# Kernel optimization log

Measured on AMD Instinct MI355X. Metric: run time of the kernel, lower is better.

## Reference

```python
import jax, jax.numpy as jnp
import numpy as np

H = 32        # query heads
HKV = 8       # kv heads
D = 64        # head_dim
EPS = 1e-6    # rms_norm_eps
LAYER_IDX = 8
LAMBDA_INIT = float(0.8 - 0.6 * np.exp(-0.3 * LAYER_IDX))
NEG = -1e9


def rotate_half(x):
    x1, x2 = jnp.split(x, 2, axis=-1)
    return jnp.concatenate([-x2, x1], axis=-1)


def setup_inputs() -> dict:
    key = jax.random.key(0)
    ks = jax.random.split(key, 10)
    B, S, HID = 1, 2048, 2048
    hidden_states = jax.random.normal(ks[0], (B, S, HID), jnp.float32)
    # rotary embeddings (HF llama style): cos/sin [S, D]
    inv_freq = 1.0 / (10000.0 ** (np.arange(0, D, 2, dtype=np.float64) / D))
    freqs = np.outer(np.arange(S, dtype=np.float64), inv_freq)
    emb = np.concatenate([freqs, freqs], axis=-1)
    cos = jnp.asarray(np.cos(emb), jnp.float32)
    sin = jnp.asarray(np.sin(emb), jnp.float32)
    w = 0.02
    Wq = w * jax.random.normal(ks[1], (H * D, HID), jnp.float32)
    Wk = w * jax.random.normal(ks[2], (HKV * D, HID), jnp.float32)
    Wv = w * jax.random.normal(ks[3], (HKV * D, HID), jnp.float32)
    Wo = w * jax.random.normal(ks[4], (HID, H * D), jnp.float32)
    lam_std = 0.1
    lambda_q1 = lam_std * jax.random.normal(ks[5], (D,), jnp.float32)
    lambda_k1 = lam_std * jax.random.normal(ks[6], (D,), jnp.float32)
    lambda_q2 = lam_std * jax.random.normal(ks[7], (D,), jnp.float32)
    lambda_k2 = lam_std * jax.random.normal(ks[8], (D,), jnp.float32)
    return dict(hidden_states=hidden_states, cos=cos, sin=sin, Wq=Wq, Wk=Wk,
                Wv=Wv, Wo=Wo, lambda_q1=lambda_q1, lambda_k1=lambda_k1,
                lambda_q2=lambda_q2, lambda_k2=lambda_k2)


def reference(hidden_states, cos, sin, Wq, Wk, Wv, Wo,
              lambda_q1, lambda_k1, lambda_q2, lambda_k2):
    B, S, _ = hidden_states.shape
    # projections -> [B, H, S, D]
    q = (hidden_states @ Wq.T).reshape(B, S, H, D).transpose(0, 2, 1, 3)
    k = (hidden_states @ Wk.T).reshape(B, S, HKV, D).transpose(0, 2, 1, 3)
    v = (hidden_states @ Wv.T).reshape(B, S, HKV, D).transpose(0, 2, 1, 3)
    # RoPE (cos/sin broadcast over batch/head dims)
    q = q * cos + rotate_half(q) * sin
    k = k * cos + rotate_half(k) * sin
    # GQA repeat_kv: each kv head repeated consecutively
    g = H // HKV
    k = jnp.repeat(k, g, axis=1)
    v = jnp.repeat(v, g, axis=1)
    # differential value: concat first/second half of heads along feature dim
    v_cat = jnp.concatenate([v[:, :H // 2], v[:, H // 2:]], axis=-1)  # [B,H/2,S,2D]
    v_rep = jnp.tile(v_cat, (1, 2, 1, 1))                              # [B,H,S,2D]
    # causal attention (flash-attn is_causal, dropout=0 at eval)
    scores = jnp.einsum('bhqd,bhkd->bhqk', q, k) / np.sqrt(D)
    causal = jnp.tril(jnp.ones((S, S), bool))
    scores = jnp.where(causal, scores, NEG)
    probs = jax.nn.softmax(scores.astype(jnp.float32), axis=-1).astype(q.dtype)
    out = jnp.einsum('bhqk,bhkd->bhqd', probs, v_rep)  # [B,H,S,2D]
    out1, out2 = out[:, :H // 2], out[:, H // 2:]
    lam1 = jnp.exp(jnp.sum(lambda_q1 * lambda_k1))
    lam2 = jnp.exp(jnp.sum(lambda_q2 * lambda_k2))
    lam = lam1 - lam2 + LAMBDA_INIT
    a = out1 - lam * out2                               # [B,H/2,S,2D]
    # RMSNorm over 2D, no affine
    a = a * jax.lax.rsqrt(jnp.mean(a * a, axis=-1, keepdims=True) + EPS)
    a = (1.0 - LAMBDA_INIT) * a
    a = a.transpose(0, 2, 1, 3).reshape(B, S, H * D)
    return a @ Wo.T
```

## Files before the change

kernel.cpp:

```cpp
#include <hip/hip_runtime.h>

typedef unsigned short u16;
typedef __attribute__((ext_vector_type(8))) short v8s;
typedef __attribute__((ext_vector_type(4))) float v4f;

#define S_LEN 2048
#define HID   2048
#define NH    32
#define NKV   8
#define HD    64
#define DVV   128
#define LAMBDA_INIT  0.7455692280263525f
#define ONE_MINUS_LI 0.2544307719736475f

__device__ __forceinline__ u16 f2b(float f){
  union { float f; unsigned int i; } v; v.f = f;
  unsigned int x = v.i;
  unsigned int r = (x + 0x7fffu + ((x >> 16) & 1u)) >> 16;
  return (u16)r;
}
__device__ __forceinline__ float b2f(u16 u){
  union { unsigned int i; float f; } v; v.i = ((unsigned int)u) << 16; return v.f;
}

__device__ __forceinline__ void gld16(const u16* g, u16* l){
  __builtin_amdgcn_global_load_lds(
      (const __attribute__((address_space(1))) unsigned int*)g,
      (__attribute__((address_space(3))) unsigned int*)l, 16, 0, 0);
}

__global__ __launch_bounds__(256) void cast5(
    const float* __restrict__ hs, const float* __restrict__ Wq,
    const float* __restrict__ Wk, const float* __restrict__ Wv,
    const float* __restrict__ Wo,
    u16* __restrict__ hsb, u16* __restrict__ Wqkvb, u16* __restrict__ Wob)
{
  int b = blockIdx.x;
  const float* S; u16* D; int rb;
  if (b < 2048)      { S = hs; D = hsb;             rb = b; }
  else if (b < 4096) { S = Wq; D = Wqkvb;           rb = b - 2048; }
  else if (b < 4608) { S = Wk; D = Wqkvb + 4194304; rb = b - 4096; }
  else if (b < 5120) { S = Wv; D = Wqkvb + 5242880; rb = b - 4608; }
  else               { S = Wo; D = Wob;             rb = b - 5120; }
  size_t i = ((size_t)rb * 256 + threadIdx.x) * 8;
  float4 a = *(const float4*)(S + i);
  float4 c = *(const float4*)(S + i + 4);
  u16 o[8] = {f2b(a.x), f2b(a.y), f2b(a.z), f2b(a.w), f2b(c.x), f2b(c.y), f2b(c.z), f2b(c.w)};
  *(uint4*)(D + i) = *(const uint4*)o;
}

template<int OUT_BF16>
__global__ __launch_bounds__(256) void gemm_bf16(const u16* __restrict__ A, const u16* __restrict__ B,
                                                 void* __restrict__ Cv, int M, int N, int K)
{
  __shared__ __attribute__((aligned(16))) u16 As[128*64];
  __shared__ __attribute__((aligned(16))) u16 Bs[128*64];
  const int t    = threadIdx.x;
  const int w    = t >> 6, lane = t & 63;
  const int mm   = lane & 15, g = lane >> 4;
  const int wr   = w >> 1, wc = w & 1;
  const int m0   = blockIdx.y * 128, n0 = blockIdx.x * 128;
  const int srow = w*32 + (lane >> 3);
  const int sch  = lane & 7;

  v4f acc[4][4];
#pragma unroll
  for (int i = 0; i < 4; i++)
#pragma unroll
    for (int j = 0; j < 4; j++) acc[i][j] = (v4f){0.f,0.f,0.f,0.f};

  for (int k0 = 0; k0 < K; k0 += 64){
    __syncthreads();
#pragma unroll
    for (int i = 0; i < 4; i++){
      int r  = srow + i*8;
      int ce = ((sch ^ (r & 7)) * 8);
      gld16(A + (size_t)(m0 + r) * K + k0 + ce, &As[w*2048 + i*512]);
      gld16(B + (size_t)(n0 + r) * K + k0 + ce, &Bs[w*2048 + i*512]);
    }
    __syncthreads();
#pragma unroll
    for (int kc = 0; kc < 2; kc++){
      v8s af[4], bf[4];
#pragma unroll
      for (int i = 0; i < 4; i++){
        int r = wr*64 + i*16 + mm;
        af[i] = *(const v8s*)&As[r*64 + (((kc*4 + g) ^ (r & 7)) * 8)];
      }
#pragma unroll
      for (int j = 0; j < 4; j++){
        int r = wc*64 + j*16 + mm;
        bf[j] = *(const v8s*)&Bs[r*64 + (((kc*4 + g) ^ (r & 7)) * 8)];
      }
#pragma unroll
      for (int i = 0; i < 4; i++)
#pragma unroll
        for (int j = 0; j < 4; j++)
          acc[i][j] = __builtin_amdgcn_mfma_f32_16x16x32_bf16(af[i], bf[j], acc[i][j], 0, 0, 0);
    }
  }
  if (OUT_BF16){
    u16* C = (u16*)Cv;
#pragma unroll
    for (int i = 0; i < 4; i++)
#pragma unroll
      for (int j = 0; j < 4; j++)
#pragma unroll
        for (int r = 0; r < 4; r++)
          C[(size_t)(m0 + wr*64 + i*16 + g*4 + r) * N + n0 + wc*64 + j*16 + mm] = f2b(acc[i][j][r]);
  } else {
    float* C = (float*)Cv;
#pragma unroll
    for (int i = 0; i < 4; i++)
#pragma unroll
      for (int j = 0; j < 4; j++)
#pragma unroll
        for (int r = 0; r < 4; r++)
          C[(size_t)(m0 + wr*64 + i*16 + g*4 + r) * N + n0 + wc*64 + j*16 + mm] = acc[i][j][r];
  }
}

__global__ __launch_bounds__(256) void rope_all(const u16* __restrict__ QKVb,
    const float* __restrict__ cosb, const float* __restrict__ sinb,
    u16* __restrict__ Qbf, u16* __restrict__ Kbf)
{
  int b = blockIdx.x;
  int d, h, s;
  const u16* src; u16* dst;
  if (b < 8192){
    int idx = b * 256 + threadIdx.x;
    d = idx & 31; h = (idx >> 5) & 31; s = idx >> 10;
    src = QKVb + (size_t)s * 3072 + h * HD + d;
    dst = Qbf + ((size_t)h * S_LEN + s) * HD + d;
  } else {
    int idx = (b - 8192) * 256 + threadIdx.x;
    d = idx & 31; h = (idx >> 5) & 7; s = idx >> 8;
    src = QKVb + (size_t)s * 3072 + 2048 + h * HD + d;
    dst = Kbf + ((size_t)h * S_LEN + s) * HD + d;
  }
  float c1 = cosb[s * HD + d],      s1 = sinb[s * HD + d];
  float c2 = cosb[s * HD + d + 32], s2 = sinb[s * HD + d + 32];
  float x1 = b2f(src[0]), x2 = b2f(src[32]);
  dst[0]  = f2b(x1 * c1 - x2 * s1);
  dst[32] = f2b(x2 * c2 + x1 * s2);
}

__global__ __launch_bounds__(256) void vtrans(const u16* __restrict__ Vb, int stride, u16* __restrict__ Vt)
{
  __shared__ u16 T[64][72];
  const int b = blockIdx.x;
  const int h = b >> 5;
  const int s0 = (b & 31) * 64;
  const int t = threadIdx.x;
#pragma unroll
  for (int i = 0; i < 4; i++){
    int u = t + i * 256;
    int r = u >> 4, c4 = (u & 15) * 4;
    uint2 v = *(const uint2*)&Vb[(size_t)(s0 + r) * stride + h * HD + c4];
    T[c4+0][r] = (u16)(v.x & 0xffff); T[c4+1][r] = (u16)(v.x >> 16);
    T[c4+2][r] = (u16)(v.y & 0xffff); T[c4+3][r] = (u16)(v.y >> 16);
  }
  __syncthreads();
#pragma unroll
  for (int i = 0; i < 2; i++){
    int u = t + i * 256;
    int d = u >> 3, ch = (u & 7) * 8;
    *(uint4*)&Vt[((size_t)h * HD + d) * S_LEN + s0 + ch] = *(const uint4*)&T[d][ch];
  }
}

__global__ __launch_bounds__(512) void attn_fused(
    const u16* __restrict__ Qbf, const u16* __restrict__ Kbf, const u16* __restrict__ Vt,
    const float* __restrict__ lq1, const float* __restrict__ lk1,
    const float* __restrict__ lq2, const float* __restrict__ lk2,
    u16* __restrict__ Ctx)
{
  __shared__ __attribute__((aligned(16))) u16 SM[41984];
  u16* QPa = SM;
  u16* QPb = SM + 4608;
  u16* Ksf = SM + 9216;
  u16* Vs  = SM + 25600;
  float* OLDS = (float*)(SM + 9216);

  const int p   = blockIdx.x;
  const int hp  = blockIdx.y;
  const int kva = hp >> 2, kvb = kva + 4;
  const int t   = threadIdx.x, w = t >> 6, lane = t & 63;
  const int hb  = w >> 2;
  const int wq  = w & 3;
  const int mm  = lane & 15, g = lane >> 4, g8 = g * 8;
  const int sr  = t >> 3;
  const int sc  = t & 7;
  const int so  = sc * 8;
  const int x0  = ((g ^ (mm & 7)) * 8);
  const int x1  = (((g + 4) ^ (mm & 7)) * 8);

  u16* QP = hb ? QPb : QPa;

  float lp1 = lq1[lane] * lk1[lane];
  float lp2 = lq2[lane] * lk2[lane];
#pragma unroll
  for (int off = 1; off < 64; off <<= 1){
    lp1 += __shfl_xor(lp1, off);
    lp2 += __shfl_xor(lp2, off);
  }
  const float lam = __expf(lp1) - __expf(lp2) + LAMBDA_INIT;

  for (int seg = 0; seg < 2; seg++){
    const int qt = seg ? p : (31 - p);
    const int q0 = qt * 64;

    __syncthreads();
    {
      int ce = ((sc ^ (sr & 7)) * 8);
      gld16(Kbf + ((size_t)kva * S_LEN + sr) * HD + ce, Ksf + (w*8)*64);
      gld16(Kbf + ((size_t)kvb * S_LEN + sr) * HD + ce, Ksf + 8192 + (w*8)*64);
      gld16(Vt + ((size_t)kva * HD + sr) * S_LEN + ce, Vs + (w*8)*64);
      gld16(Vt + ((size_t)kvb * HD + sr) * S_LEN + ce, Vs + (w*8 + 64)*64);
    }
    *(uint4*)&QPa[sr*72 + so] = *(const uint4*)&Qbf[((size_t)hp        * S_LEN + q0 + sr) * HD + so];
    *(uint4*)&QPb[sr*72 + so] = *(const uint4*)&Qbf[((size_t)(hp + 16) * S_LEN + q0 + sr) * HD + so];
    __syncthreads();
    v8s qa0 = *(const v8s*)&QP[(wq*16 + mm)*72 + g8];
    v8s qa1 = *(const v8s*)&QP[(wq*16 + mm)*72 + 32 + g8];

    v4f O[8];
#pragma unroll
    for (int n = 0; n < 8; n++) O[n] = (v4f){0.f,0.f,0.f,0.f};
    float l[4] = {0.f,0.f,0.f,0.f};

    for (int k0 = 0; k0 <= q0; k0 += 64){
      const int cur = (k0 >> 6) & 1;
      if (k0){
        asm volatile("s_waitcnt vmcnt(0)" ::: "memory");
        __builtin_amdgcn_s_barrier();
        __builtin_amdgcn_sched_barrier(0);
      }
      if (k0 + 64 <= q0){
        int ce = ((sc ^ (sr & 7)) * 8);
        gld16(Vt + ((size_t)kva * HD + sr) * S_LEN + k0 + 64 + ce, Vs + (cur^1)*8192 + (w*8)*64);
        gld16(Vt + ((size_t)kvb * HD + sr) * S_LEN + k0 + 64 + ce, Vs + (cur^1)*8192 + (w*8 + 64)*64);
        gld16(Kbf + ((size_t)kva * S_LEN + k0 + 64 + sr) * HD + ce, Ksf + (cur^1)*4096 + (w*8)*64);
        gld16(Kbf + ((size_t)kvb * S_LEN + k0 + 64 + sr) * HD + ce, Ksf + 8192 + (cur^1)*4096 + (w*8)*64);
      }

      const u16* Kh = Ksf + hb*8192 + cur*4096;
      const bool dg = (k0 == q0);
      v4f S[4];
#pragma unroll
      for (int n = 0; n < 4; n++){
        int row = n*16 + mm;
        v8s kb0 = *(const v8s*)&Kh[row*64 + x0];
        v8s kb1 = *(const v8s*)&Kh[row*64 + x1];
        v4f z = (v4f){0.f,0.f,0.f,0.f};
        z = __builtin_amdgcn_mfma_f32_16x16x32_bf16(qa0, kb0, z, 0, 0, 0);
        z = __builtin_amdgcn_mfma_f32_16x16x32_bf16(qa1, kb1, z, 0, 0, 0);
        S[n] = z;
      }
#pragma unroll
      for (int n = 0; n < 4; n++)
#pragma unroll
        for (int r = 0; r < 4; r++){
          float pe = __expf(S[n][r] * 0.125f);
          if (dg && (n*16 + mm > wq*16 + g*4 + r)) pe = 0.f;
          l[r] += pe;
          QP[(wq*16 + g*4 + r)*72 + n*16 + mm] = f2b(pe);
        }
      v8s pa0 = *(const v8s*)&QP[(wq*16 + mm)*72 + g8];
      v8s pa1 = *(const v8s*)&QP[(wq*16 + mm)*72 + 32 + g8];
      const u16* Vh = Vs + cur*8192;
#pragma unroll
      for (int n = 0; n < 8; n++){
        int row = n*16 + mm;
        v8s vb0 = *(const v8s*)&Vh[row*64 + x0];
        v8s vb1 = *(const v8s*)&Vh[row*64 + x1];
        O[n] = __builtin_amdgcn_mfma_f32_16x16x32_bf16(pa0, vb0, O[n], 0, 0, 0);
        O[n] = __builtin_amdgcn_mfma_f32_16x16x32_bf16(pa1, vb1, O[n], 0, 0, 0);
      }
    }

#pragma unroll
    for (int off = 1; off < 16; off <<= 1)
#pragma unroll
      for (int r = 0; r < 4; r++)
        l[r] += __shfl_xor(l[r], off);
    float il[4];
#pragma unroll
    for (int r = 0; r < 4; r++) il[r] = hb ? (lam / l[r]) : (1.0f / l[r]);

    __syncthreads();
    if (hb){
#pragma unroll
      for (int n = 0; n < 8; n++)
#pragma unroll
        for (int r = 0; r < 4; r++)
          OLDS[(wq*16 + g*4 + r)*128 + n*16 + mm] = O[n][r] * il[r];
    }
    __syncthreads();
    if (!hb){
      float av[8][4];
      float ss[4] = {0.f,0.f,0.f,0.f};
#pragma unroll
      for (int n = 0; n < 8; n++)
#pragma unroll
        for (int r = 0; r < 4; r++){
          float a = O[n][r] * il[r] - OLDS[(wq*16 + g*4 + r)*128 + n*16 + mm];
          av[n][r] = a;
          ss[r] += a * a;
        }
#pragma unroll
      for (int off = 1; off < 16; off <<= 1)
#pragma unroll
        for (int r = 0; r < 4; r++)
          ss[r] += __shfl_xor(ss[r], off);
      float rv[4];
#pragma unroll
      for (int r = 0; r < 4; r++)
        rv[r] = rsqrtf(ss[r] * (1.0f/128.0f) + 1e-6f) * ONE_MINUS_LI;
#pragma unroll
      for (int n = 0; n < 8; n++)
#pragma unroll
        for (int r = 0; r < 4; r++){
          int srow = q0 + wq*16 + g*4 + r;
          Ctx[(size_t)srow * HID + hp * DVV + n*16 + mm] = f2b(av[n][r] * rv[r]);
        }
    }
  }
}

extern "C" void kernel_launch(void* const* d_in, const int* in_sizes, int n_in,
                              void* d_out, int out_size, void* d_ws, size_t ws_size,
                              hipStream_t stream)
{
  (void)in_sizes; (void)n_in; (void)out_size; (void)ws_size;
  const float* hs   = (const float*)d_in[0];
  const float* cosb = (const float*)d_in[1];
  const float* sinb = (const float*)d_in[2];
  const float* Wq   = (const float*)d_in[3];
  const float* Wk   = (const float*)d_in[4];
  const float* Wv   = (const float*)d_in[5];
  const float* Wo   = (const float*)d_in[6];
  const float* lq1  = (const float*)d_in[7];
  const float* lk1  = (const float*)d_in[8];
  const float* lq2  = (const float*)d_in[9];
  const float* lk2  = (const float*)d_in[10];

  char* ws = (char*)d_ws;
  u16* hsb   = (u16*)(ws);
  u16* Wqkvb = (u16*)(ws + (8u  << 20));
  u16* QKVb  = (u16*)(ws + (20u << 20));
  u16* Ctx   = (u16*)(ws + (20u << 20));
  u16* Wob   = (u16*)(ws + (32u << 20));
  u16* Kbf   = (u16*)(ws + (44u << 20));
  u16* Vt    = (u16*)(ws + (46u << 20));
  u16* Qbf   = (u16*)(ws + (48u << 20));

  cast5<<<7168, 256, 0, stream>>>(hs, Wq, Wk, Wv, Wo, hsb, Wqkvb, Wob);
  gemm_bf16<1><<<dim3(24, 16), 256, 0, stream>>>(hsb, Wqkvb, QKVb, S_LEN, 3072, HID);
  rope_all<<<10240, 256, 0, stream>>>(QKVb, cosb, sinb, Qbf, Kbf);
  vtrans<<<NKV * (S_LEN/64), 256, 0, stream>>>(QKVb + 2560, 3072, Vt);
  attn_fused<<<dim3(16, 16), 512, 0, stream>>>(Qbf, Kbf, Vt, lq1, lk1, lq2, lk2, Ctx);
  gemm_bf16<0><<<dim3(16, 16), 256, 0, stream>>>(Ctx, Wob, (float*)d_out, S_LEN, 2048, HID);
}
```

Measured before the change: 253.6 us.

## Replace paired query-tile scheduling with 128-row tiles using 1024-thread blocks

```diff
diff --git a/kernel.cpp b/kernel.cpp
--- a/kernel.cpp
+++ b/kernel.cpp
@@ -169,31 +169,36 @@
   }
 }
 
-__global__ __launch_bounds__(512) void attn_fused(
+__global__ __launch_bounds__(1024, 4) void attn_fused(
     const u16* __restrict__ Qbf, const u16* __restrict__ Kbf, const u16* __restrict__ Vt,
     const float* __restrict__ lq1, const float* __restrict__ lk1,
     const float* __restrict__ lq2, const float* __restrict__ lk2,
     u16* __restrict__ Ctx)
 {
-  __shared__ __attribute__((aligned(16))) u16 SM[41984];
+  __shared__ __attribute__((aligned(16))) u16 SM[51200];
   u16* QPa = SM;
-  u16* QPb = SM + 4608;
-  u16* Ksf = SM + 9216;
-  u16* Vs  = SM + 25600;
-  float* OLDS = (float*)(SM + 9216);
-
-  const int p   = blockIdx.x;
+  u16* QPb = SM + 9216;
+  u16* Ksf = SM + 18432;
+  u16* Vs  = SM + 34816;
+  float* OLDS = (float*)(SM + 18432);
+
+  const int d   = blockIdx.x;
   const int hp  = blockIdx.y;
   const int kva = hp >> 2, kvb = kva + 4;
   const int t   = threadIdx.x, w = t >> 6, lane = t & 63;
-  const int hb  = w >> 2;
-  const int wq  = w & 3;
+  const int hb  = w >> 3;
+  const int wq  = w & 7;
   const int mm  = lane & 15, g = lane >> 4, g8 = g * 8;
   const int sr  = t >> 3;
   const int sc  = t & 7;
   const int so  = sc * 8;
   const int x0  = ((g ^ (mm & 7)) * 8);
   const int x1  = (((g + 4) ^ (mm & 7)) * 8);
+  const int khd  = (sr >> 6) ? kvb : kva;
+  const int rloc = sr & 63;
+  const int ce   = ((sc ^ (sr & 7)) * 8);
+  u16* kdst = Ksf + (w >> 3) * 8192 + ((w & 7) * 8) * 64;
+  u16* vdst = Vs + (w * 8) * 64;
 
   u16* QP = hb ? QPb : QPa;
 
@@ -206,125 +211,115 @@
   }
   const float lam = __expf(lp1) - __expf(lp2) + LAMBDA_INIT;
 
-  for (int seg = 0; seg < 2; seg++){
-    const int qt = seg ? p : (31 - p);
-    const int q0 = qt * 64;
-
-    __syncthreads();
-    {
-      int ce = ((sc ^ (sr & 7)) * 8);
-      gld16(Kbf + ((size_t)kva * S_LEN + sr) * HD + ce, Ksf + (w*8)*64);
-      gld16(Kbf + ((size_t)kvb * S_LEN + sr) * HD + ce, Ksf + 8192 + (w*8)*64);
-      gld16(Vt + ((size_t)kva * HD + sr) * S_LEN + ce, Vs + (w*8)*64);
-      gld16(Vt + ((size_t)kvb * HD + sr) * S_LEN + ce, Vs + (w*8 + 64)*64);
-    }
-    *(uint4*)&QPa[sr*72 + so] = *(const uint4*)&Qbf[((size_t)hp        * S_LEN + q0 + sr) * HD + so];
-    *(uint4*)&QPb[sr*72 + so] = *(const uint4*)&Qbf[((size_t)(hp + 16) * S_LEN + q0 + sr) * HD + so];
-    __syncthreads();
-    v8s qa0 = *(const v8s*)&QP[(wq*16 + mm)*72 + g8];
-    v8s qa1 = *(const v8s*)&QP[(wq*16 + mm)*72 + 32 + g8];
-
-    v4f O[8];
-#pragma unroll
-    for (int n = 0; n < 8; n++) O[n] = (v4f){0.f,0.f,0.f,0.f};
-    float l[4] = {0.f,0.f,0.f,0.f};
-
-    for (int k0 = 0; k0 <= q0; k0 += 64){
-      const int cur = (k0 >> 6) & 1;
-      if (k0){
-        asm volatile("s_waitcnt vmcnt(0)" ::: "memory");
-        __builtin_amdgcn_s_barrier();
-        __builtin_amdgcn_sched_barrier(0);
-      }
-      if (k0 + 64 <= q0){
-        int ce = ((sc ^ (sr & 7)) * 8);
-        gld16(Vt + ((size_t)kva * HD + sr) * S_LEN + k0 + 64 + ce, Vs + (cur^1)*8192 + (w*8)*64);
-        gld16(Vt + ((size_t)kvb * HD + sr) * S_LEN + k0 + 64 + ce, Vs + (cur^1)*8192 + (w*8 + 64)*64);
-        gld16(Kbf + ((size_t)kva * S_LEN + k0 + 64 + sr) * HD + ce, Ksf + (cur^1)*4096 + (w*8)*64);
-        gld16(Kbf + ((size_t)kvb * S_LEN + k0 + 64 + sr) * HD + ce, Ksf + 8192 + (cur^1)*4096 + (w*8)*64);
-      }
-
-      const u16* Kh = Ksf + hb*8192 + cur*4096;
-      const bool dg = (k0 == q0);
-      v4f S[4];
-#pragma unroll
-      for (int n = 0; n < 4; n++){
-        int row = n*16 + mm;
-        v8s kb0 = *(const v8s*)&Kh[row*64 + x0];
-        v8s kb1 = *(const v8s*)&Kh[row*64 + x1];
-        v4f z = (v4f){0.f,0.f,0.f,0.f};
-        z = __builtin_amdgcn_mfma_f32_16x16x32_bf16(qa0, kb0, z, 0, 0, 0);
-        z = __builtin_amdgcn_mfma_f32_16x16x32_bf16(qa1, kb1, z, 0, 0, 0);
-        S[n] = z;
-      }
-#pragma unroll
-      for (int n = 0; n < 4; n++)
-#pragma unroll
-        for (int r = 0; r < 4; r++){
-          float pe = __expf(S[n][r] * 0.125f);
-          if (dg && (n*16 + mm > wq*16 + g*4 + r)) pe = 0.f;
-          l[r] += pe;
-          QP[(wq*16 + g*4 + r)*72 + n*16 + mm] = f2b(pe);
-        }
-      v8s pa0 = *(const v8s*)&QP[(wq*16 + mm)*72 + g8];
-      v8s pa1 = *(const v8s*)&QP[(wq*16 + mm)*72 + 32 + g8];
-      const u16* Vh = Vs + cur*8192;
-#pragma unroll
-      for (int n = 0; n < 8; n++){
-        int row = n*16 + mm;
-        v8s vb0 = *(const v8s*)&Vh[row*64 + x0];
-        v8s vb1 = *(const v8s*)&Vh[row*64 + x1];
-        O[n] = __builtin_amdgcn_mfma_f32_16x16x32_bf16(pa0, vb0, O[n], 0, 0, 0);
-        O[n] = __builtin_amdgcn_mfma_f32_16x16x32_bf16(pa1, vb1, O[n], 0, 0, 0);
-      }
-    }
-
+  const int q0   = d * 128;
+  const int kmax = q0 + 64;
+
+  gld16(Kbf + ((size_t)khd * S_LEN + rloc) * HD + ce, kdst);
+  gld16(Vt  + ((size_t)khd * HD + rloc) * S_LEN + ce, vdst);
+  *(uint4*)&QPa[sr*72 + so] = *(const uint4*)&Qbf[((size_t)hp        * S_LEN + q0 + sr) * HD + so];
+  *(uint4*)&QPb[sr*72 + so] = *(const uint4*)&Qbf[((size_t)(hp + 16) * S_LEN + q0 + sr) * HD + so];
+  __syncthreads();
+  v8s qa0 = *(const v8s*)&QP[(wq*16 + mm)*72 + g8];
+  v8s qa1 = *(const v8s*)&QP[(wq*16 + mm)*72 + 32 + g8];
+
+  v4f O[8];
+#pragma unroll
+  for (int n = 0; n < 8; n++) O[n] = (v4f){0.f,0.f,0.f,0.f};
+  float l[4] = {0.f,0.f,0.f,0.f};
+
+  for (int k0 = 0; k0 <= kmax; k0 += 64){
+    const int cur = (k0 >> 6) & 1;
+    if (k0){
+      asm volatile("s_waitcnt vmcnt(0)" ::: "memory");
+      __builtin_amdgcn_s_barrier();
+      __builtin_amdgcn_sched_barrier(0);
+    }
+    if (k0 + 64 <= kmax){
+      gld16(Vt  + ((size_t)khd * HD + rloc) * S_LEN + k0 + 64 + ce, vdst + (cur^1)*8192);
+      gld16(Kbf + ((size_t)khd * S_LEN + k0 + 64 + rloc) * HD + ce, kdst + (cur^1)*4096);
+    }
+
+    const u16* Kh = Ksf + hb*8192 + cur*4096;
+    const int kof = k0 - q0;
+    const bool dg = (kof >= 0);
+    v4f S[4];
+#pragma unroll
+    for (int n = 0; n < 4; n++){
+      int row = n*16 + mm;
+      v8s kb0 = *(const v8s*)&Kh[row*64 + x0];
+      v8s kb1 = *(const v8s*)&Kh[row*64 + x1];
+      v4f z = (v4f){0.f,0.f,0.f,0.f};
+      z = __builtin_amdgcn_mfma_f32_16x16x32_bf16(qa0, kb0, z, 0, 0, 0);
+      z = __builtin_amdgcn_mfma_f32_16x16x32_bf16(qa1, kb1, z, 0, 0, 0);
+      S[n] = z;
+    }
+#pragma unroll
+    for (int n = 0; n < 4; n++)
+#pragma unroll
+      for (int r = 0; r < 4; r++){
+        float pe = __expf(S[n][r] * 0.125f);
+        if (dg && (kof + n*16 + mm > wq*16 + g*4 + r)) pe = 0.f;
+        l[r] += pe;
+        QP[(wq*16 + g*4 + r)*72 + n*16 + mm] = f2b(pe);
+      }
+    v8s pa0 = *(const v8s*)&QP[(wq*16 + mm)*72 + g8];
+    v8s pa1 = *(const v8s*)&QP[(wq*16 + mm)*72 + 32 + g8];
+    const u16* Vh = Vs + cur*8192;
+#pragma unroll
+    for (int n = 0; n < 8; n++){
+      int row = n*16 + mm;
+      v8s vb0 = *(const v8s*)&Vh[row*64 + x0];
+      v8s vb1 = *(const v8s*)&Vh[row*64 + x1];
+      O[n] = __builtin_amdgcn_mfma_f32_16x16x32_bf16(pa0, vb0, O[n], 0, 0, 0);
+      O[n] = __builtin_amdgcn_mfma_f32_16x16x32_bf16(pa1, vb1, O[n], 0, 0, 0);
+    }
+  }
+
+#pragma unroll
+  for (int off = 1; off < 16; off <<= 1)
+#pragma unroll
+    for (int r = 0; r < 4; r++)
+      l[r] += __shfl_xor(l[r], off);
+  float il[4];
+#pragma unroll
+  for (int r = 0; r < 4; r++) il[r] = hb ? (lam / l[r]) : (1.0f / l[r]);
+
+  __syncthreads();
+  if (hb){
+#pragma unroll
+    for (int n = 0; n < 8; n++)
+#pragma unroll
+      for (int r = 0; r < 4; r++)
+        OLDS[(wq*16 + g*4 + r)*128 + n*16 + mm] = O[n][r] * il[r];
+  }
+  __syncthreads();
+  if (!hb){
+    float av[8][4];
+    float ss[4] = {0.f,0.f,0.f,0.f};
+#pragma unroll
+    for (int n = 0; n < 8; n++)
+#pragma unroll
+      for (int r = 0; r < 4; r++){
+        float a = O[n][r] * il[r] - OLDS[(wq*16 + g*4 + r)*128 + n*16 + mm];
+        av[n][r] = a;
+        ss[r] += a * a;
+      }
 #pragma unroll
     for (int off = 1; off < 16; off <<= 1)
 #pragma unroll
       for (int r = 0; r < 4; r++)
-        l[r] += __shfl_xor(l[r], off);
-    float il[4];
-#pragma unroll
-    for (int r = 0; r < 4; r++) il[r] = hb ? (lam / l[r]) : (1.0f / l[r]);
-
-    __syncthreads();
-    if (hb){
-#pragma unroll
-      for (int n = 0; n < 8; n++)
-#pragma unroll
-        for (int r = 0; r < 4; r++)
-          OLDS[(wq*16 + g*4 + r)*128 + n*16 + mm] = O[n][r] * il[r];
-    }
-    __syncthreads();
-    if (!hb){
-      float av[8][4];
-      float ss[4] = {0.f,0.f,0.f,0.f};
-#pragma unroll
-      for (int n = 0; n < 8; n++)
-#pragma unroll
-        for (int r = 0; r < 4; r++){
-          float a = O[n][r] * il[r] - OLDS[(wq*16 + g*4 + r)*128 + n*16 + mm];
-          av[n][r] = a;
-          ss[r] += a * a;
-        }
-#pragma unroll
-      for (int off = 1; off < 16; off <<= 1)
-#pragma unroll
-        for (int r = 0; r < 4; r++)
-          ss[r] += __shfl_xor(ss[r], off);
-      float rv[4];
-#pragma unroll
-      for (int r = 0; r < 4; r++)
-        rv[r] = rsqrtf(ss[r] * (1.0f/128.0f) + 1e-6f) * ONE_MINUS_LI;
-#pragma unroll
-      for (int n = 0; n < 8; n++)
-#pragma unroll
-        for (int r = 0; r < 4; r++){
-          int srow = q0 + wq*16 + g*4 + r;
-          Ctx[(size_t)srow * HID + hp * DVV + n*16 + mm] = f2b(av[n][r] * rv[r]);
-        }
-    }
+        ss[r] += __shfl_xor(ss[r], off);
+    float rv[4];
+#pragma unroll
+    for (int r = 0; r < 4; r++)
+      rv[r] = rsqrtf(ss[r] * (1.0f/128.0f) + 1e-6f) * ONE_MINUS_LI;
+#pragma unroll
+    for (int n = 0; n < 8; n++)
+#pragma unroll
+      for (int r = 0; r < 4; r++){
+        int srow = q0 + wq*16 + g*4 + r;
+        Ctx[(size_t)srow * HID + hp * DVV + n*16 + mm] = f2b(av[n][r] * rv[r]);
+      }
   }
 }
 
@@ -359,6 +354,6 @@
   gemm_bf16<1><<<dim3(24, 16), 256, 0, stream>>>(hsb, Wqkvb, QKVb, S_LEN, 3072, HID);
   rope_all<<<10240, 256, 0, stream>>>(QKVb, cosb, sinb, Qbf, Kbf);
   vtrans<<<NKV * (S_LEN/64), 256, 0, stream>>>(QKVb + 2560, 3072, Vt);
-  attn_fused<<<dim3(16, 16), 512, 0, stream>>>(Qbf, Kbf, Vt, lq1, lk1, lq2, lk2, Ctx);
+  attn_fused<<<dim3(16, 16), 1024, 0, stream>>>(Qbf, Kbf, Vt, lq1, lk1, lq2, lk2, Ctx);
   gemm_bf16<0><<<dim3(16, 16), 256, 0, stream>>>(Ctx, Wob, (float*)d_out, S_LEN, 2048, HID);
 }
```

Measured after the change: 271.3 us. 7.0% more time.

## Process two KV tiles per barrier with four-slot shared-memory ring

Applied to the files above, without the earlier changes.

```diff
diff --git a/kernel.cpp b/kernel.cpp
--- a/kernel.cpp
+++ b/kernel.cpp
@@ -175,11 +175,11 @@
     const float* __restrict__ lq2, const float* __restrict__ lk2,
     u16* __restrict__ Ctx)
 {
-  __shared__ __attribute__((aligned(16))) u16 SM[41984];
+  __shared__ __attribute__((aligned(16))) u16 SM[74752];
   u16* QPa = SM;
   u16* QPb = SM + 4608;
   u16* Ksf = SM + 9216;
-  u16* Vs  = SM + 25600;
+  u16* Vs  = SM + 41984;
   float* OLDS = (float*)(SM + 9216);
 
   const int p   = blockIdx.x;
@@ -194,6 +194,7 @@
   const int so  = sc * 8;
   const int x0  = ((g ^ (mm & 7)) * 8);
   const int x1  = (((g + 4) ^ (mm & 7)) * 8);
+  const int ce  = ((sc ^ (sr & 7)) * 8);
 
   u16* QP = hb ? QPb : QPa;
 
@@ -206,18 +207,57 @@
   }
   const float lam = __expf(lp1) - __expf(lp2) + LAMBDA_INIT;
 
+#define TILE_ISSUE(kk) do { \
+    const int tb_ = ((kk) >> 6) & 3; \
+    gld16(Vt  + ((size_t)kva * HD + sr) * S_LEN + (kk) + ce, Vs + tb_*8192 + (w*8)*64); \
+    gld16(Vt  + ((size_t)kvb * HD + sr) * S_LEN + (kk) + ce, Vs + tb_*8192 + (w*8 + 64)*64); \
+    gld16(Kbf + ((size_t)kva * S_LEN + (kk) + sr) * HD + ce, Ksf + tb_*4096 + (w*8)*64); \
+    gld16(Kbf + ((size_t)kvb * S_LEN + (kk) + sr) * HD + ce, Ksf + 16384 + tb_*4096 + (w*8)*64); \
+  } while(0)
+
+#define TILE_COMPUTE(kk, dgf) do { \
+    const int tb_ = ((kk) >> 6) & 3; \
+    const u16* Kh_ = Ksf + hb*16384 + tb_*4096; \
+    v4f S_[4]; \
+    _Pragma("unroll") \
+    for (int n = 0; n < 4; n++){ \
+      int row = n*16 + mm; \
+      v8s kb0 = *(const v8s*)&Kh_[row*64 + x0]; \
+      v8s kb1 = *(const v8s*)&Kh_[row*64 + x1]; \
+      v4f z = (v4f){0.f,0.f,0.f,0.f}; \
+      z = __builtin_amdgcn_mfma_f32_16x16x32_bf16(qa0, kb0, z, 0, 0, 0); \
+      z = __builtin_amdgcn_mfma_f32_16x16x32_bf16(qa1, kb1, z, 0, 0, 0); \
+      S_[n] = z; \
+    } \
+    _Pragma("unroll") \
+    for (int n = 0; n < 4; n++) \
+      _Pragma("unroll") \
+      for (int r = 0; r < 4; r++){ \
+        float pe = __expf(S_[n][r] * 0.125f); \
+        if ((dgf) && (n*16 + mm > wq*16 + g*4 + r)) pe = 0.f; \
+        l[r] += pe; \
+        QP[(wq*16 + g*4 + r)*72 + n*16 + mm] = f2b(pe); \
+      } \
+    v8s pa0 = *(const v8s*)&QP[(wq*16 + mm)*72 + g8]; \
+    v8s pa1 = *(const v8s*)&QP[(wq*16 + mm)*72 + 32 + g8]; \
+    const u16* Vh_ = Vs + tb_*8192; \
+    _Pragma("unroll") \
+    for (int n = 0; n < 8; n++){ \
+      int row = n*16 + mm; \
+      v8s vb0 = *(const v8s*)&Vh_[row*64 + x0]; \
+      v8s vb1 = *(const v8s*)&Vh_[row*64 + x1]; \
+      O[n] = __builtin_amdgcn_mfma_f32_16x16x32_bf16(pa0, vb0, O[n], 0, 0, 0); \
+      O[n] = __builtin_amdgcn_mfma_f32_16x16x32_bf16(pa1, vb1, O[n], 0, 0, 0); \
+    } \
+  } while(0)
+
   for (int seg = 0; seg < 2; seg++){
     const int qt = seg ? p : (31 - p);
     const int q0 = qt * 64;
 
     __syncthreads();
-    {
-      int ce = ((sc ^ (sr & 7)) * 8);
-      gld16(Kbf + ((size_t)kva * S_LEN + sr) * HD + ce, Ksf + (w*8)*64);
-      gld16(Kbf + ((size_t)kvb * S_LEN + sr) * HD + ce, Ksf + 8192 + (w*8)*64);
-      gld16(Vt + ((size_t)kva * HD + sr) * S_LEN + ce, Vs + (w*8)*64);
-      gld16(Vt + ((size_t)kvb * HD + sr) * S_LEN + ce, Vs + (w*8 + 64)*64);
-    }
+    TILE_ISSUE(0);
+    if (64 <= q0) TILE_ISSUE(64);
     *(uint4*)&QPa[sr*72 + so] = *(const uint4*)&Qbf[((size_t)hp        * S_LEN + q0 + sr) * HD + so];
     *(uint4*)&QPb[sr*72 + so] = *(const uint4*)&Qbf[((size_t)(hp + 16) * S_LEN + q0 + sr) * HD + so];
     __syncthreads();
@@ -229,54 +269,25 @@
     for (int n = 0; n < 8; n++) O[n] = (v4f){0.f,0.f,0.f,0.f};
     float l[4] = {0.f,0.f,0.f,0.f};
 
-    for (int k0 = 0; k0 <= q0; k0 += 64){
-      const int cur = (k0 >> 6) & 1;
+    int k0 = 0;
+    for (; k0 + 64 <= q0; k0 += 128){
       if (k0){
         asm volatile("s_waitcnt vmcnt(0)" ::: "memory");
         __builtin_amdgcn_s_barrier();
         __builtin_amdgcn_sched_barrier(0);
       }
-      if (k0 + 64 <= q0){
-        int ce = ((sc ^ (sr & 7)) * 8);
-        gld16(Vt + ((size_t)kva * HD + sr) * S_LEN + k0 + 64 + ce, Vs + (cur^1)*8192 + (w*8)*64);
-        gld16(Vt + ((size_t)kvb * HD + sr) * S_LEN + k0 + 64 + ce, Vs + (cur^1)*8192 + (w*8 + 64)*64);
-        gld16(Kbf + ((size_t)kva * S_LEN + k0 + 64 + sr) * HD + ce, Ksf + (cur^1)*4096 + (w*8)*64);
-        gld16(Kbf + ((size_t)kvb * S_LEN + k0 + 64 + sr) * HD + ce, Ksf + 8192 + (cur^1)*4096 + (w*8)*64);
+      if (k0 + 128 <= q0) TILE_ISSUE(k0 + 128);
+      if (k0 + 192 <= q0) TILE_ISSUE(k0 + 192);
+      TILE_COMPUTE(k0, false);
+      TILE_COMPUTE(k0 + 64, (k0 + 64 == q0));
+    }
+    if (k0 <= q0){
+      if (k0){
+        asm volatile("s_waitcnt vmcnt(0)" ::: "memory");
+        __builtin_amdgcn_s_barrier();
+        __builtin_amdgcn_sched_barrier(0);
       }
-
-      const u16* Kh = Ksf + hb*8192 + cur*4096;
-      const bool dg = (k0 == q0);
-      v4f S[4];
-#pragma unroll
-      for (int n = 0; n < 4; n++){
-        int row = n*16 + mm;
-        v8s kb0 = *(const v8s*)&Kh[row*64 + x0];
-        v8s kb1 = *(const v8s*)&Kh[row*64 + x1];
-        v4f z = (v4f){0.f,0.f,0.f,0.f};
-        z = __builtin_amdgcn_mfma_f32_16x16x32_bf16(qa0, kb0, z, 0, 0, 0);
-        z = __builtin_amdgcn_mfma_f32_16x16x32_bf16(qa1, kb1, z, 0, 0, 0);
-        S[n] = z;
-      }
-#pragma unroll
-      for (int n = 0; n < 4; n++)
-#pragma unroll
-        for (int r = 0; r < 4; r++){
-          float pe = __expf(S[n][r] * 0.125f);
-          if (dg && (n*16 + mm > wq*16 + g*4 + r)) pe = 0.f;
-          l[r] += pe;
-          QP[(wq*16 + g*4 + r)*72 + n*16 + mm] = f2b(pe);
-        }
-      v8s pa0 = *(const v8s*)&QP[(wq*16 + mm)*72 + g8];
-      v8s pa1 = *(const v8s*)&QP[(wq*16 + mm)*72 + 32 + g8];
-      const u16* Vh = Vs + cur*8192;
-#pragma unroll
-      for (int n = 0; n < 8; n++){
-        int row = n*16 + mm;
-        v8s vb0 = *(const v8s*)&Vh[row*64 + x0];
-        v8s vb1 = *(const v8s*)&Vh[row*64 + x1];
-        O[n] = __builtin_amdgcn_mfma_f32_16x16x32_bf16(pa0, vb0, O[n], 0, 0, 0);
-        O[n] = __builtin_amdgcn_mfma_f32_16x16x32_bf16(pa1, vb1, O[n], 0, 0, 0);
-      }
+      TILE_COMPUTE(k0, true);
     }
 
 #pragma unroll
@@ -326,6 +337,8 @@
         }
     }
   }
+#undef TILE_ISSUE
+#undef TILE_COMPUTE
 }
 
 extern "C" void kernel_launch(void* const* d_in, const int* in_sizes, int n_in,
```

Result: no change. 251.5 us (-0.8%).

## Double-buffer GEMM LDS tiles and raise wave priority around attention MFMAs

Applied to the files above, without the earlier changes.

```diff
diff --git a/kernel.cpp b/kernel.cpp
--- a/kernel.cpp
+++ b/kernel.cpp
@@ -53,8 +53,8 @@
 __global__ __launch_bounds__(256) void gemm_bf16(const u16* __restrict__ A, const u16* __restrict__ B,
                                                  void* __restrict__ Cv, int M, int N, int K)
 {
-  __shared__ __attribute__((aligned(16))) u16 As[128*64];
-  __shared__ __attribute__((aligned(16))) u16 Bs[128*64];
+  __shared__ __attribute__((aligned(16))) u16 As[2][128*64];
+  __shared__ __attribute__((aligned(16))) u16 Bs[2][128*64];
   const int t    = threadIdx.x;
   const int w    = t >> 6, lane = t & 63;
   const int mm   = lane & 15, g = lane >> 4;
@@ -69,28 +69,40 @@
 #pragma unroll
     for (int j = 0; j < 4; j++) acc[i][j] = (v4f){0.f,0.f,0.f,0.f};
 
+#define G_STAGE(kk, buf) do { \
+    _Pragma("unroll") \
+    for (int i = 0; i < 4; i++){ \
+      int r  = srow + i*8; \
+      int ce = ((sch ^ (r & 7)) * 8); \
+      gld16(A + (size_t)(m0 + r) * K + (kk) + ce, &As[buf][w*2048 + i*512]); \
+      gld16(B + (size_t)(n0 + r) * K + (kk) + ce, &Bs[buf][w*2048 + i*512]); \
+    } \
+  } while(0)
+
+  G_STAGE(0, 0);
+  __syncthreads();
+
   for (int k0 = 0; k0 < K; k0 += 64){
-    __syncthreads();
-#pragma unroll
-    for (int i = 0; i < 4; i++){
-      int r  = srow + i*8;
-      int ce = ((sch ^ (r & 7)) * 8);
-      gld16(A + (size_t)(m0 + r) * K + k0 + ce, &As[w*2048 + i*512]);
-      gld16(B + (size_t)(n0 + r) * K + k0 + ce, &Bs[w*2048 + i*512]);
-    }
-    __syncthreads();
+    const int cur = (k0 >> 6) & 1;
+    if (k0){
+      asm volatile("s_waitcnt vmcnt(0)" ::: "memory");
+      __builtin_amdgcn_s_barrier();
+      __builtin_amdgcn_sched_barrier(0);
+    }
+    if (k0 + 64 < K) G_STAGE(k0 + 64, cur ^ 1);
+
 #pragma unroll
     for (int kc = 0; kc < 2; kc++){
       v8s af[4], bf[4];
 #pragma unroll
       for (int i = 0; i < 4; i++){
         int r = wr*64 + i*16 + mm;
-        af[i] = *(const v8s*)&As[r*64 + (((kc*4 + g) ^ (r & 7)) * 8)];
+        af[i] = *(const v8s*)&As[cur][r*64 + (((kc*4 + g) ^ (r & 7)) * 8)];
       }
 #pragma unroll
       for (int j = 0; j < 4; j++){
         int r = wc*64 + j*16 + mm;
-        bf[j] = *(const v8s*)&Bs[r*64 + (((kc*4 + g) ^ (r & 7)) * 8)];
+        bf[j] = *(const v8s*)&Bs[cur][r*64 + (((kc*4 + g) ^ (r & 7)) * 8)];
       }
 #pragma unroll
       for (int i = 0; i < 4; i++)
@@ -99,6 +111,8 @@
           acc[i][j] = __builtin_amdgcn_mfma_f32_16x16x32_bf16(af[i], bf[j], acc[i][j], 0, 0, 0);
     }
   }
+#undef G_STAGE
+
   if (OUT_BF16){
     u16* C = (u16*)Cv;
 #pragma unroll
@@ -247,6 +261,7 @@
       const u16* Kh = Ksf + hb*8192 + cur*4096;
       const bool dg = (k0 == q0);
       v4f S[4];
+      __builtin_amdgcn_s_setprio(1);
 #pragma unroll
       for (int n = 0; n < 4; n++){
         int row = n*16 + mm;
@@ -257,6 +272,7 @@
         z = __builtin_amdgcn_mfma_f32_16x16x32_bf16(qa1, kb1, z, 0, 0, 0);
         S[n] = z;
       }
+      __builtin_amdgcn_s_setprio(0);
 #pragma unroll
       for (int n = 0; n < 4; n++)
 #pragma unroll
@@ -269,6 +285,7 @@
       v8s pa0 = *(const v8s*)&QP[(wq*16 + mm)*72 + g8];
       v8s pa1 = *(const v8s*)&QP[(wq*16 + mm)*72 + 32 + g8];
       const u16* Vh = Vs + cur*8192;
+      __builtin_amdgcn_s_setprio(1);
 #pragma unroll
       for (int n = 0; n < 8; n++){
         int row = n*16 + mm;
@@ -277,6 +294,7 @@
         O[n] = __builtin_amdgcn_mfma_f32_16x16x32_bf16(pa0, vb0, O[n], 0, 0, 0);
         O[n] = __builtin_amdgcn_mfma_f32_16x16x32_bf16(pa1, vb1, O[n], 0, 0, 0);
       }
+      __builtin_amdgcn_s_setprio(0);
     }
 
 #pragma unroll
```

Measured after the change: 245.0 us. 1.03x faster.
